# Performance work log

Hardware: AMD Instinct MI355X
Metric: run time of the kernel (lower is better)

The kernel has to match this reference:

```python
import jax, jax.numpy as jnp
import numpy as np

# Sizes: B graphs of N nodes each, K nearest neighbours, D=feat_dim=nhid, C=pos_dim
B, N, K, D, C = 4, 1024, 128, 32, 2
L = 3                     # number of EGNN conv layers
E_IN = 2 * D + 1          # edge MLP input: feats_i | feats_j | rel_dist (edge_dim=0, fourier=0)
E_H = 2 * E_IN            # edge MLP hidden


def _lin(key, fan_in, fan_out):
    kw, kb = jax.random.split(key)
    w = jax.random.normal(kw, (fan_in, fan_out), jnp.float32) / np.sqrt(fan_in)
    b = jax.random.normal(kb, (fan_out,), jnp.float32) * 0.01
    return w, b


def _stack(key, fan_in, fan_out):
    ws, bs = zip(*[_lin(k, fan_in, fan_out) for k in jax.random.split(key, L)])
    return jnp.stack(ws), jnp.stack(bs)


def setup_inputs() -> dict:
    key = jax.random.key(0)
    ks = jax.random.split(key, 10)
    feat_ = jax.random.normal(ks[0], (B * N, D), jnp.float32)
    coor_ = jax.random.normal(ks[1], (B * N, C), jnp.float32)
    batch = jnp.full((B,), N, dtype=jnp.int32)   # per-graph node counts (equal-size graphs)
    embed_w, embed_b = _lin(ks[2], D, D)         # embed: Linear(feat_dim, nhid)
    e1_w, e1_b = _stack(ks[3], E_IN, E_H)        # edge MLP
    e2_w, e2_b = _stack(ks[4], E_H, D)           # -> m_dim = nhid
    gate_w, gate_b = _stack(ks[5], D, 1)         # soft_edges gate
    c1_w, c1_b = _stack(ks[6], D, 4 * D)         # coors MLP
    c2_w, c2_b = _stack(ks[7], 4 * D, 1)
    n1_w, n1_b = _stack(ks[8], 2 * D, 2 * D)     # node MLP
    n2_w, n2_b = _stack(ks[9], 2 * D, D)
    coors_scale = jnp.full((L, 1), 1e-2, jnp.float32)  # CoorsNorm scale (init 1e-2)
    return dict(feat_=feat_, coor_=coor_, batch=batch, embed_w=embed_w, embed_b=embed_b,
                e1_w=e1_w, e1_b=e1_b, e2_w=e2_w, e2_b=e2_b, gate_w=gate_w, gate_b=gate_b,
                c1_w=c1_w, c1_b=c1_b, c2_w=c2_w, c2_b=c2_b, n1_w=n1_w, n1_b=n1_b,
                n2_w=n2_w, n2_b=n2_b, coors_scale=coors_scale)


def _lrelu(x):
    return jax.nn.leaky_relu(x, 0.1)


def _gather(x, idx):
    # x: [B, n, d], idx: [B, n, k] -> [B, n, k, d]
    return jax.vmap(lambda xb, ib: xb[ib])(x, idx)


def _egnn_layer(feats, coors, p):
    (e1_w, e1_b, e2_w, e2_b, gate_w, gate_b, c1_w, c1_b, c2_w, c2_b,
     n1_w, n1_b, n2_w, n2_b, scale) = p
    # pairwise squared distances; k smallest (self included, valid_radius=inf)
    diff = coors[:, :, None, :] - coors[:, None, :, :]      # [B,n,n,C]
    dist = jnp.sum(diff * diff, axis=-1)                    # [B,n,n]
    neg_d, idx = jax.lax.top_k(-dist, K)                    # k nearest
    rel_dist = -neg_d[..., None]                            # [B,n,K,1]
    rel_coors = coors[:, :, None, :] - _gather(coors, idx)  # [B,n,K,C]
    feats_j = _gather(feats, idx)                           # [B,n,K,D]
    feats_i = jnp.broadcast_to(feats[:, :, None, :], feats_j.shape)
    edge_in = jnp.concatenate([feats_i, feats_j, rel_dist], axis=-1)  # [B,n,K,E_IN]
    # edge MLP: Lin -> act -> Lin -> act ; soft edge gate
    m = _lrelu(_lrelu(edge_in @ e1_w + e1_b) @ e2_w + e2_b)            # [B,n,K,D]
    m = m * jax.nn.sigmoid(m @ gate_w + gate_b)
    # coordinate update: coors_mlp -> scalar weights; CoorsNorm on rel coords
    cw = (_lrelu(m @ c1_w + c1_b) @ c2_w + c2_b)[..., 0]               # [B,n,K]
    norm = jnp.maximum(jnp.linalg.norm(rel_coors, axis=-1, keepdims=True), 1e-8)
    rel_n = rel_coors / norm * scale
    coors_out = jnp.einsum('bik,bikc->bic', cw, rel_n) + coors
    # feature update: sum-pool messages, node MLP with residual
    m_i = jnp.sum(m, axis=2)                                           # [B,n,D]
    node_in = jnp.concatenate([feats, m_i], axis=-1)
    feats_out = _lrelu(node_in @ n1_w + n1_b) @ n2_w + n2_b + feats
    return feats_out, coors_out


def reference(feat_, coor_, batch, embed_w, embed_b, e1_w, e1_b, e2_w, e2_b,
              gate_w, gate_b, c1_w, c1_b, c2_w, c2_b, n1_w, n1_b, n2_w, n2_b,
              coors_scale):
    # embed MLP (dropout is identity at p=0 / eval), then batch equal-size graphs
    feats = _lrelu(feat_ @ embed_w + embed_b).reshape(B, N, D)
    coors = coor_.reshape(B, N, C)
    for l in range(L):
        p = (e1_w[l], e1_b[l], e2_w[l], e2_b[l], gate_w[l], gate_b[l],
             c1_w[l], c1_b[l], c2_w[l], c2_b[l], n1_w[l], n1_b[l],
             n2_w[l], n2_b[l], coors_scale[l])
        feats, coors = _egnn_layer(feats, coors, p)
    return feats.reshape(B * N, D)
```

## Files before the change

kernel.cpp:

```cpp
#include <hip/hip_runtime.h>
#include <hip/hip_bf16.h>
#include <math.h>

#define BB 4
#define NN 1024
#define KK 128
#define DD 32
#define LL 3
#define EH 130
#define EHP 132

typedef float f32x4 __attribute__((ext_vector_type(4)));
typedef short s16x8 __attribute__((ext_vector_type(8)));

__device__ __forceinline__ float lrelu(float x) { return fmaxf(x, 0.1f * x); }

__device__ __forceinline__ unsigned pk2(float a, float b) {
    __hip_bfloat162 h = __float22bfloat162_rn(float2{a, b});
    return *(unsigned*)&h;
}
__device__ __forceinline__ unsigned short bf16_hu(float v) {
    return (unsigned short)((__float_as_uint(v) + 0x8000u) >> 16);
}
__device__ __forceinline__ unsigned short bf16_rne(float v) {
    unsigned u = __float_as_uint(v);
    return (unsigned short)((u + 0x7fffu + ((u >> 16) & 1u)) >> 16);
}

__device__ __forceinline__ void knn_select(const float2* __restrict__ cbp, int i, int lane,
                                           unsigned* __restrict__ hist,
                                           int* __restrict__ nb) {
    const float2 ci = cbp[i];
    unsigned k[16];
#pragma unroll
    for (int s = 0; s < 16; s++) {
        float2 cj = cbp[lane + 64 * s];
        float dx = ci.x - cj.x, dy = ci.y - cj.y;
        float d = __fadd_rn(__fmul_rn(dx, dx), __fmul_rn(dy, dy));
        k[s] = __float_as_uint(d);
    }
    unsigned prefix = 0u;
    unsigned r = KK - 1;
#pragma unroll
    for (int pass = 0; pass < 4; pass++) {
        const int sh = 24 - 8 * pass;
        const unsigned mpref = (pass == 0) ? 0u : (0xFFFFFFFFu << (sh + 8));
        ((uint4*)hist)[lane] = uint4{0u, 0u, 0u, 0u};
        __threadfence_block();
#pragma unroll
        for (int s = 0; s < 16; s++) {
            if ((k[s] & mpref) == prefix)
                atomicAdd(&hist[(k[s] >> sh) & 255u], 1u);
        }
        __threadfence_block();
        const uint4 h = ((const uint4*)hist)[lane];
        const unsigned partial = h.x + h.y + h.z + h.w;
        unsigned incl = partial;
#pragma unroll
        for (int off = 1; off < 64; off <<= 1) {
            unsigned v = __shfl_up(incl, off, 64);
            if (lane >= off) incl += v;
        }
        const unsigned excl = incl - partial;
        const bool own = (r >= excl) && (r < incl);
        unsigned enc = 0u;
        if (own) {
            unsigned hh[4] = {h.x, h.y, h.z, h.w};
            unsigned e = excl;
            int bin = -1;
#pragma unroll
            for (int ii = 0; ii < 4; ii++) {
                if (bin < 0) {
                    if (r < e + hh[ii]) bin = ii;
                    else e += hh[ii];
                }
            }
            enc = (((unsigned)(4 * lane + bin)) << 16) | (r - e);
        }
        const unsigned long long mk = __ballot(own);
        const int src = __ffsll((unsigned long long)mk) - 1;
        enc = __shfl(enc, src, 64);
        prefix |= (enc >> 16) << sh;
        r = enc & 0xFFFFu;
    }
    const unsigned dstar = prefix;

    const unsigned long long below = (1ull << lane) - 1ull;
    unsigned run = 0;
#pragma unroll
    for (int s = 0; s < 16; s++) {
        unsigned long long m = __ballot(k[s] < dstar);
        if (k[s] < dstar) nb[run + (unsigned)__popcll(m & below)] = lane + 64 * s;
        run += (unsigned)__popcll(m);
    }
    const int need = KK - (int)run;
    unsigned tie = 0;
    for (int s = 0; s < 16 && (int)tie < need; s++) {
        unsigned long long m = __ballot(k[s] == dstar);
        if (k[s] == dstar) {
            unsigned r2 = tie + (unsigned)__popcll(m & below);
            if ((int)r2 < need) nb[run + r2] = lane + 64 * s;
        }
        tie += (unsigned)__popcll(m);
    }
}

__global__ __launch_bounds__(128) void prep_kernel(
    const float* __restrict__ feat,
    const float* __restrict__ ew, const float* __restrict__ eb,
    float* __restrict__ fout,
    const float* __restrict__ e1w0, const float* __restrict__ e1b0,
    float* __restrict__ HI, float* __restrict__ HJ,
    const float* __restrict__ e2w, const float* __restrict__ e2b,
    const float* __restrict__ c1w,
    unsigned short* __restrict__ e2f, unsigned short* __restrict__ c1f) {
    const int bid = blockIdx.x;
    const int t = threadIdx.x;
    if (bid < 2048) {
        __shared__ float sfe[2][DD];
        const int n0 = bid * 2;
        if (t < 64) {
            const int nl = t >> 5, o = t & 31;
            const float* f = feat + (size_t)(n0 + nl) * DD;
            float a = eb[o];
#pragma unroll
            for (int k = 0; k < DD; k++) a = fmaf(f[k], ew[k * DD + o], a);
            a = lrelu(a);
            fout[(size_t)(n0 + nl) * DD + o] = a;
            sfe[nl][o] = a;
        }
        __syncthreads();
        for (int idx = t; idx < 2 * EHP; idx += 128) {
            const int nl = idx / EHP, o = idx - nl * EHP;
            const size_t off = (size_t)(n0 + nl) * EHP + o;
            if (o >= EH) { HI[off] = 0.f; HJ[off] = 0.f; continue; }
            const float* fl = sfe[nl];
            float aa = e1b0[o], cc = 0.f;
#pragma unroll
            for (int k = 0; k < DD; k++) aa = fmaf(fl[k], e1w0[k * EH + o], aa);
#pragma unroll
            for (int k = 0; k < DD; k++) cc = fmaf(fl[k], e1w0[(DD + k) * EH + o], cc);
            HI[off] = aa;
            HJ[off] = cc;
        }
    } else {
        const int TOT_E2 = LL * 5120;
        const int TOT = TOT_E2 + LL * 4096;
        for (int u = (bid - 2048) * 128 + t; u < TOT; u += 96 * 128) {
            if (u < TOT_E2) {
                int l = u / 5120, v = u - l * 5120;
                int jj = v & 7, la = (v >> 3) & 63, nt = (v >> 9) & 1, c = v >> 10;
                int n = nt * 16 + (la & 15);
                float val;
                if (c < 4) {
                    int k = 32 * c + (la >> 4) * 8 + jj;
                    val = e2w[(size_t)l * EH * DD + k * DD + n];
                } else {
                    int ks = (la >> 4) * 8 + jj;
                    val = (ks == 0) ? e2w[((size_t)l * EH + 128) * DD + n]
                        : (ks == 1) ? e2w[((size_t)l * EH + 129) * DD + n]
                        : (ks == 2) ? e2b[(size_t)l * DD + n] : 0.f;
                }
                e2f[u] = bf16_rne(val);
            } else {
                int v = u - TOT_E2;
                int jj = v & 7, la = (v >> 3) & 63, nt = (v >> 9) & 7, l = v >> 12;
                int k = (la >> 4) * 8 + jj;
                int n = nt * 16 + (la & 15);
                c1f[v] = bf16_rne(c1w[(size_t)l * DD * 128 + k * 128 + n]);
            }
        }
    }
}

__global__ __launch_bounds__(256) void layer_kernel(
    const float* __restrict__ feats_in, const float* __restrict__ coors_in,
    const float* __restrict__ HI, const float* __restrict__ HJ,
    const float* __restrict__ w65,
    const unsigned short* __restrict__ e2f,
    const unsigned short* __restrict__ c1f,
    const float* __restrict__ gw, const float* __restrict__ gb,
    const float* __restrict__ c1b, const float* __restrict__ c2w, const float* __restrict__ c2b,
    const float* __restrict__ n1w, const float* __restrict__ n1b,
    const float* __restrict__ n2w, const float* __restrict__ n2b,
    const float* __restrict__ scale,
    const float* __restrict__ e1wn, const float* __restrict__ e1bn,
    float* __restrict__ HIn, float* __restrict__ HJn,
    float* __restrict__ feats_out, float* __restrict__ coors_out) {
    const int node = blockIdx.x;
    const int b = node >> 10;
    const int t = threadIdx.x;
    const int lane = t & 63, wid = t >> 6;
    const int ln = lane & 15, q = lane >> 4;
    const int rowbase = wid * 32;

    __shared__ __align__(16) float shi[EHP];
    __shared__ __align__(16) float sw65[EHP];
    __shared__ __align__(16) unsigned short smA[4 * 32 * 32];
    __shared__ float sx0[128], sx1[128], su[128], sv[128], srd[128];
    __shared__ int snb[128];
    __shared__ float sgw[DD], sfi[DD], sfo[DD];
    __shared__ float sc1b[128], sc2w[128];
    __shared__ float redm[4][DD], redc[4][2];
    __shared__ float sni[2 * DD], shd[2 * DD];
    __shared__ float sp1[4][2 * DD], sp2[4][DD];

    if (t < 64) {
        knn_select((const float2*)coors_in + (size_t)b * NN, node & (NN - 1), lane,
                   (unsigned*)smA, snb);
    } else {
        for (int u = t - 64; u < EHP; u += 192) {
            shi[u] = HI[(size_t)node * EHP + u];
            sw65[u] = (u < EH) ? w65[u] : 0.f;
        }
        if (t - 64 < DD) { sfi[t - 64] = feats_in[node * DD + (t - 64)]; sgw[t - 64] = gw[t - 64]; }
        if (t >= 128) { sc1b[t - 128] = c1b[t - 128]; sc2w[t - 128] = c2w[t - 128]; }
    }
    __syncthreads();

    const float cix = coors_in[node * 2], ciy = coors_in[node * 2 + 1];
    if (t < 128) {
        const int j = snb[t];
        const float2 cj = *(const float2*)(coors_in + ((size_t)(b * NN) + j) * 2);
        const float dx = cix - cj.x, dy = ciy - cj.y;
        const float rd = __fadd_rn(__fmul_rn(dx, dx), __fmul_rn(dy, dy));
        srd[t] = rd;
        const float nrm = fmaxf(sqrtf(rd), 1e-8f);
        const float s = scale[0] / nrm;
        su[t] = dx * s;
        sv[t] = dy * s;
        const float2 hjt = *(const float2*)(HJ + ((size_t)(b * NN) + j) * EHP + 128);
        sx0[t] = lrelu(shi[128] + hjt.x + rd * sw65[128]);
        sx1[t] = lrelu(shi[129] + hjt.y + rd * sw65[129]);
    }
    __syncthreads();

    float rdR[2];
    const float* hjb[2];
#pragma unroll
    for (int mt = 0; mt < 2; mt++) {
        const int row = rowbase + mt * 16 + ln;
        rdR[mt] = srd[row];
        hjb[mt] = HJ + ((size_t)(b * NN) + snb[row]) * EHP;
    }

    const float4* shi4 = (const float4*)shi;
    const float4* sw4  = (const float4*)sw65;

    const f32x4 zz = {0.f, 0.f, 0.f, 0.f};
    f32x4 accA[2][2];
    accA[0][0] = zz; accA[0][1] = zz; accA[1][0] = zz; accA[1][1] = zz;

    float4 ha[2], hbv[2];
#pragma unroll
    for (int mt = 0; mt < 2; mt++) {
        const float4* hjp = (const float4*)(hjb[mt] + q * 8);
        ha[mt] = hjp[0];
        hbv[mt] = hjp[1];
    }
    s16x8 bcur0 = *(const s16x8*)(e2f + (0 * 64 + lane) * 8);
    s16x8 bcur1 = *(const s16x8*)(e2f + (1 * 64 + lane) * 8);

#pragma unroll 1
    for (int c = 0; c < 4; c++) {
        s16x8 bn0 = *(const s16x8*)(e2f + (((c + 1) * 2 + 0) * 64 + lane) * 8);
        s16x8 bn1 = *(const s16x8*)(e2f + (((c + 1) * 2 + 1) * 64 + lane) * 8);
        float4 nha[2], nhb[2];
        if (c < 3) {
#pragma unroll
            for (int mt = 0; mt < 2; mt++) {
                const float4* hjp = (const float4*)(hjb[mt] + (c + 1) * 32 + q * 8);
                nha[mt] = hjp[0];
                nhb[mt] = hjp[1];
            }
        }
        const int kb = c * 8 + q * 2;
        const float4 hi0 = shi4[kb], hi1 = shi4[kb + 1];
        const float4 wv0 = sw4[kb],  wv1 = sw4[kb + 1];
#pragma unroll
        for (int mt = 0; mt < 2; mt++) {
            const float r = rdR[mt];
            union { s16x8 v; unsigned u[4]; } A;
            A.u[0] = pk2(lrelu(hi0.x + ha[mt].x + r * wv0.x), lrelu(hi0.y + ha[mt].y + r * wv0.y));
            A.u[1] = pk2(lrelu(hi0.z + ha[mt].z + r * wv0.z), lrelu(hi0.w + ha[mt].w + r * wv0.w));
            A.u[2] = pk2(lrelu(hi1.x + hbv[mt].x + r * wv1.x), lrelu(hi1.y + hbv[mt].y + r * wv1.y));
            A.u[3] = pk2(lrelu(hi1.z + hbv[mt].z + r * wv1.z), lrelu(hi1.w + hbv[mt].w + r * wv1.w));
            accA[mt][0] = __builtin_amdgcn_mfma_f32_16x16x32_bf16(A.v, bcur0, accA[mt][0], 0, 0, 0);
            accA[mt][1] = __builtin_amdgcn_mfma_f32_16x16x32_bf16(A.v, bcur1, accA[mt][1], 0, 0, 0);
        }
#pragma unroll
        for (int mt = 0; mt < 2; mt++) { ha[mt] = nha[mt]; hbv[mt] = nhb[mt]; }
        bcur0 = bn0; bcur1 = bn1;
    }

    {
#pragma unroll
        for (int mt = 0; mt < 2; mt++) {
            const int row = rowbase + mt * 16 + ln;
            union { s16x8 v; unsigned u[4]; } A;
            const unsigned p0 = pk2(sx0[row], sx1[row]);
            A.u[0] = (q == 0) ? p0 : 0u;
            A.u[1] = (q == 0) ? 0x00003f80u : 0u;
            A.u[2] = 0u;
            A.u[3] = 0u;
            accA[mt][0] = __builtin_amdgcn_mfma_f32_16x16x32_bf16(A.v, bcur0, accA[mt][0], 0, 0, 0);
            accA[mt][1] = __builtin_amdgcn_mfma_f32_16x16x32_bf16(A.v, bcur1, accA[mt][1], 0, 0, 0);
        }
    }

    s16x8 cfr[8];
#pragma unroll
    for (int g8 = 0; g8 < 8; g8++)
        cfr[g8] = *(const s16x8*)(c1f + (g8 * 64 + lane) * 8);

#pragma unroll
    for (int mt = 0; mt < 2; mt++)
#pragma unroll
        for (int nt = 0; nt < 2; nt++)
#pragma unroll
            for (int r = 0; r < 4; r++)
                accA[mt][nt][r] = lrelu(accA[mt][nt][r]);

    const float gbv = gb[0];
#pragma unroll
    for (int mt = 0; mt < 2; mt++) {
        float p[4];
#pragma unroll
        for (int r = 0; r < 4; r++)
            p[r] = accA[mt][0][r] * sgw[ln] + accA[mt][1][r] * sgw[16 + ln];
#pragma unroll
        for (int off = 1; off <= 8; off <<= 1)
#pragma unroll
            for (int r = 0; r < 4; r++) p[r] += __shfl_xor(p[r], off);
#pragma unroll
        for (int r = 0; r < 4; r++) {
            const float g = 1.f / (1.f + __expf(-(p[r] + gbv)));
            accA[mt][0][r] *= g;
            accA[mt][1][r] *= g;
        }
    }

    float mi0 = 0.f, mi1 = 0.f;
#pragma unroll
    for (int mt = 0; mt < 2; mt++)
#pragma unroll
        for (int r = 0; r < 4; r++) { mi0 += accA[mt][0][r]; mi1 += accA[mt][1][r]; }
    mi0 += __shfl_xor(mi0, 16); mi0 += __shfl_xor(mi0, 32);
    mi1 += __shfl_xor(mi1, 16); mi1 += __shfl_xor(mi1, 32);
    if (lane < 16) { redm[wid][lane] = mi0; redm[wid][16 + lane] = mi1; }

    __syncthreads();
    unsigned short* smw = smA + wid * (32 * 32);
#pragma unroll
    for (int mt = 0; mt < 2; mt++)
#pragma unroll
        for (int nt = 0; nt < 2; nt++)
#pragma unroll
            for (int r = 0; r < 4; r++) {
                const int prow = (r << 3) | (4 * mt + q);
                smw[prow * 32 + nt * 16 + ln] = bf16_hu(accA[mt][nt][r]);
            }

    s16x8 a4[2];
#pragma unroll
    for (int mt = 0; mt < 2; mt++) {
        const int prow = ((ln & 3) << 3) | (4 * mt + (ln >> 2));
        a4[mt] = *(const s16x8*)(smw + prow * 32 + q * 8);
    }

    float cacc[2][4];
#pragma unroll
    for (int mt = 0; mt < 2; mt++)
#pragma unroll
        for (int r = 0; r < 4; r++) cacc[mt][r] = 0.f;

#pragma unroll
    for (int g = 0; g < 4; g++) {
        const float cb0 = sc1b[(2 * g + 0) * 16 + ln];
        const float cb1 = sc1b[(2 * g + 1) * 16 + ln];
        const f32x4 ci0 = {cb0, cb0, cb0, cb0};
        const f32x4 ci1 = {cb1, cb1, cb1, cb1};
        f32x4 c20[2], c21[2];
#pragma unroll
        for (int mt = 0; mt < 2; mt++) {
            c20[mt] = __builtin_amdgcn_mfma_f32_16x16x32_bf16(a4[mt], cfr[2 * g + 0], ci0, 0, 0, 0);
            c21[mt] = __builtin_amdgcn_mfma_f32_16x16x32_bf16(a4[mt], cfr[2 * g + 1], ci1, 0, 0, 0);
        }
#pragma unroll
        for (int h = 0; h < 2; h++) {
            const float c2wv = sc2w[(2 * g + h) * 16 + ln];
#pragma unroll
            for (int mt = 0; mt < 2; mt++)
#pragma unroll
                for (int r = 0; r < 4; r++) {
                    const float v = (h ? c21[mt][r] : c20[mt][r]);
                    cacc[mt][r] = fmaf(lrelu(v), c2wv, cacc[mt][r]);
                }
        }
    }
#pragma unroll
    for (int off = 1; off <= 8; off <<= 1)
#pragma unroll
        for (int mt = 0; mt < 2; mt++)
#pragma unroll
            for (int r = 0; r < 4; r++) cacc[mt][r] += __shfl_xor(cacc[mt][r], off);

    const float c2bv = c2b[0];
    float vxp = 0.f, vyp = 0.f;
    if (ln == 0) {
#pragma unroll
        for (int mt = 0; mt < 2; mt++)
#pragma unroll
            for (int r = 0; r < 4; r++) {
                const int row = rowbase + mt * 16 + q * 4 + r;
                const float cw = cacc[mt][r] + c2bv;
                vxp = fmaf(cw, su[row], vxp);
                vyp = fmaf(cw, sv[row], vyp);
            }
    }
    vxp += __shfl_xor(vxp, 16); vxp += __shfl_xor(vxp, 32);
    vyp += __shfl_xor(vyp, 16); vyp += __shfl_xor(vyp, 32);
    if (lane == 0) { redc[wid][0] = vxp; redc[wid][1] = vyp; }

    __syncthreads();
    if (t < DD) {
        sni[t] = sfi[t];
        sni[DD + t] = redm[0][t] + redm[1][t] + redm[2][t] + redm[3][t];
    }
    __syncthreads();
    {
        const int o = t & 63, p = t >> 6;
        float a = 0.f;
#pragma unroll
        for (int k = 0; k < 16; k++) a = fmaf(sni[p * 16 + k], n1w[(p * 16 + k) * 64 + o], a);
        sp1[p][o] = a;
    }
    __syncthreads();
    if (t < 2 * DD)
        shd[t] = lrelu(n1b[t] + ((sp1[0][t] + sp1[1][t]) + (sp1[2][t] + sp1[3][t])));
    __syncthreads();
    if (t < 128) {
        const int o = t & 31, p = t >> 5;
        float a = 0.f;
#pragma unroll
        for (int k = 0; k < 16; k++) a = fmaf(shd[p * 16 + k], n2w[(p * 16 + k) * DD + o], a);
        sp2[p][o] = a;
    }
    __syncthreads();
    if (t < DD) {
        const float val = n2b[t] + ((sp2[0][t] + sp2[1][t]) + (sp2[2][t] + sp2[3][t])) + sfi[t];
        feats_out[node * DD + t] = val;
        sfo[t] = val;
    }
    if (t == 0) {
        coors_out[node * 2]     = cix + redc[0][0] + redc[1][0] + redc[2][0] + redc[3][0];
        coors_out[node * 2 + 1] = ciy + redc[0][1] + redc[1][1] + redc[2][1] + redc[3][1];
    }
    __syncthreads();

    if (e1wn) {
        for (int idx = t; idx < 2 * EHP; idx += 256) {
            const int nl = idx / EHP, o = idx - nl * EHP;
            float* dst = (nl ? HJn : HIn) + (size_t)node * EHP + o;
            if (o >= EH) { *dst = 0.f; continue; }
            const int rowoff = nl ? DD : 0;
            float a = nl ? 0.f : e1bn[o];
#pragma unroll
            for (int k = 0; k < DD; k++) a = fmaf(sfo[k], e1wn[(rowoff + k) * EH + o], a);
            *dst = a;
        }
    }
}

extern "C" void kernel_launch(void* const* d_in, const int* in_sizes, int n_in,
                              void* d_out, int out_size, void* d_ws, size_t ws_size,
                              hipStream_t stream) {
    const float* feat_   = (const float*)d_in[0];
    const float* coor_   = (const float*)d_in[1];
    const float* embed_w = (const float*)d_in[3];
    const float* embed_b = (const float*)d_in[4];
    const float* e1_w    = (const float*)d_in[5];
    const float* e1_b    = (const float*)d_in[6];
    const float* e2_w    = (const float*)d_in[7];
    const float* e2_b    = (const float*)d_in[8];
    const float* gate_w  = (const float*)d_in[9];
    const float* gate_b  = (const float*)d_in[10];
    const float* c1_w    = (const float*)d_in[11];
    const float* c1_b    = (const float*)d_in[12];
    const float* c2_w    = (const float*)d_in[13];
    const float* c2_b    = (const float*)d_in[14];
    const float* n1_w    = (const float*)d_in[15];
    const float* n1_b    = (const float*)d_in[16];
    const float* n2_w    = (const float*)d_in[17];
    const float* n2_b    = (const float*)d_in[18];
    const float* cscale  = (const float*)d_in[19];

    float* ws = (float*)d_ws;
    float* fa   = ws;   ws += BB * NN * DD;
    float* fb   = ws;   ws += BB * NN * DD;
    float* ca   = ws;   ws += BB * NN * 2;
    float* cb2  = ws;   ws += BB * NN * 2;
    float* HI0  = ws;   ws += BB * NN * EHP;
    float* HJ0  = ws;   ws += BB * NN * EHP;
    float* HI1  = ws;   ws += BB * NN * EHP;
    float* HJ1  = ws;   ws += BB * NN * EHP;
    unsigned short* e2f = (unsigned short*)ws;
    unsigned short* c1f = e2f + LL * 5120;

    prep_kernel<<<2048 + 96, 128, 0, stream>>>(feat_, embed_w, embed_b, fa,
                                               e1_w, e1_b, HI0, HJ0,
                                               e2_w, e2_b, c1_w, e2f, c1f);

    float* HIbuf[2] = {HI0, HI1};
    float* HJbuf[2] = {HJ0, HJ1};
    const float* fin = fa;
    const float* cin = coor_;
    float* fouts[LL] = {fb, fa, (float*)d_out};
    float* couts[LL] = {ca, cb2, ca};

    for (int l = 0; l < LL; l++) {
        const int cur = l & 1, nxt = (l + 1) & 1;
        layer_kernel<<<BB * NN, 256, 0, stream>>>(
            fin, cin, HIbuf[cur], HJbuf[cur],
            e1_w + ((size_t)l * 65 + 64) * EH,
            e2f + (size_t)l * 5120,
            c1f + (size_t)l * 4096,
            gate_w + (size_t)l * DD,
            gate_b + l,
            c1_b + (size_t)l * 128,
            c2_w + (size_t)l * 128,
            c2_b + l,
            n1_w + (size_t)l * 64 * 64,
            n1_b + (size_t)l * 64,
            n2_w + (size_t)l * 64 * 32,
            n2_b + (size_t)l * DD,
            cscale + l,
            (l < LL - 1) ? (e1_w + (size_t)(l + 1) * 65 * EH) : nullptr,
            (l < LL - 1) ? (e1_b + (size_t)(l + 1) * EH) : nullptr,
            HIbuf[nxt], HJbuf[nxt],
            fouts[l], couts[l]);
        fin = fouts[l];
        cin = couts[l];
    }
}
```

Before: 328.7 us.

## Spread kNN radix selection across all four waves of the block

```diff
diff --git a/kernel.cpp b/kernel.cpp
--- a/kernel.cpp
+++ b/kernel.cpp
@@ -27,14 +27,17 @@
     return (unsigned short)((u + 0x7fffu + ((u >> 16) & 1u)) >> 16);
 }
 
-__device__ __forceinline__ void knn_select(const float2* __restrict__ cbp, int i, int lane,
-                                           unsigned* __restrict__ hist,
-                                           int* __restrict__ nb) {
+__device__ __forceinline__ void knn_block(const float2* __restrict__ cbp, int i, int t,
+                                          unsigned* __restrict__ hist,
+                                          volatile unsigned* __restrict__ scr,
+                                          int* __restrict__ nb) {
+    const int lane = t & 63, wid = t >> 6;
+    unsigned* histw = hist + wid * 256;
     const float2 ci = cbp[i];
-    unsigned k[16];
-#pragma unroll
-    for (int s = 0; s < 16; s++) {
-        float2 cj = cbp[lane + 64 * s];
+    unsigned k[4];
+#pragma unroll
+    for (int s = 0; s < 4; s++) {
+        float2 cj = cbp[wid * 256 + s * 64 + lane];
         float dx = ci.x - cj.x, dy = ci.y - cj.y;
         float d = __fadd_rn(__fmul_rn(dx, dx), __fmul_rn(dy, dy));
         k[s] = __float_as_uint(d);
@@ -45,63 +48,69 @@
     for (int pass = 0; pass < 4; pass++) {
         const int sh = 24 - 8 * pass;
         const unsigned mpref = (pass == 0) ? 0u : (0xFFFFFFFFu << (sh + 8));
-        ((uint4*)hist)[lane] = uint4{0u, 0u, 0u, 0u};
-        __threadfence_block();
-#pragma unroll
-        for (int s = 0; s < 16; s++) {
+        ((uint4*)histw)[lane] = uint4{0u, 0u, 0u, 0u};
+#pragma unroll
+        for (int s = 0; s < 4; s++) {
             if ((k[s] & mpref) == prefix)
-                atomicAdd(&hist[(k[s] >> sh) & 255u], 1u);
-        }
-        __threadfence_block();
-        const uint4 h = ((const uint4*)hist)[lane];
-        const unsigned partial = h.x + h.y + h.z + h.w;
-        unsigned incl = partial;
+                atomicAdd(&histw[(k[s] >> sh) & 255u], 1u);
+        }
+        __syncthreads();
+        unsigned tot = hist[t] + hist[256 + t] + hist[512 + t] + hist[768 + t];
+        unsigned incl = tot;
 #pragma unroll
         for (int off = 1; off < 64; off <<= 1) {
             unsigned v = __shfl_up(incl, off, 64);
             if (lane >= off) incl += v;
         }
-        const unsigned excl = incl - partial;
-        const bool own = (r >= excl) && (r < incl);
-        unsigned enc = 0u;
-        if (own) {
-            unsigned hh[4] = {h.x, h.y, h.z, h.w};
-            unsigned e = excl;
-            int bin = -1;
-#pragma unroll
-            for (int ii = 0; ii < 4; ii++) {
-                if (bin < 0) {
-                    if (r < e + hh[ii]) bin = ii;
-                    else e += hh[ii];
-                }
-            }
-            enc = (((unsigned)(4 * lane + bin)) << 16) | (r - e);
-        }
-        const unsigned long long mk = __ballot(own);
-        const int src = __ffsll((unsigned long long)mk) - 1;
-        enc = __shfl(enc, src, 64);
-        prefix |= (enc >> 16) << sh;
-        r = enc & 0xFFFFu;
+        if (lane == 63) scr[wid] = incl;
+        __syncthreads();
+        unsigned woff = 0;
+#pragma unroll
+        for (int w = 0; w < 4; w++)
+            if (w < wid) woff += scr[w];
+        incl += woff;
+        const unsigned excl = incl - tot;
+        if (r >= excl && r < incl) { scr[4] = (unsigned)t; scr[5] = r - excl; }
+        __syncthreads();
+        prefix |= scr[4] << sh;
+        r = scr[5];
     }
     const unsigned dstar = prefix;
 
     const unsigned long long below = (1ull << lane) - 1ull;
-    unsigned run = 0;
-#pragma unroll
-    for (int s = 0; s < 16; s++) {
-        unsigned long long m = __ballot(k[s] < dstar);
-        if (k[s] < dstar) nb[run + (unsigned)__popcll(m & below)] = lane + 64 * s;
-        run += (unsigned)__popcll(m);
-    }
-    const int need = KK - (int)run;
-    unsigned tie = 0;
-    for (int s = 0; s < 16 && (int)tie < need; s++) {
-        unsigned long long m = __ballot(k[s] == dstar);
+    unsigned long long mL[4], mE[4];
+    unsigned cntL = 0, cntE = 0;
+#pragma unroll
+    for (int s = 0; s < 4; s++) {
+        mL[s] = __ballot(k[s] < dstar);
+        mE[s] = __ballot(k[s] == dstar);
+        cntL += (unsigned)__popcll(mL[s]);
+        cntE += (unsigned)__popcll(mE[s]);
+    }
+    if (lane == 0) { scr[8 + wid] = cntL; scr[12 + wid] = cntE; }
+    __syncthreads();
+    unsigned offL = 0, offE = 0, totalL = 0;
+#pragma unroll
+    for (int w = 0; w < 4; w++) {
+        unsigned cl = scr[8 + w];
+        if (w < wid) { offL += cl; offE += scr[12 + w]; }
+        totalL += cl;
+    }
+    unsigned run = offL;
+#pragma unroll
+    for (int s = 0; s < 4; s++) {
+        if (k[s] < dstar) nb[run + (unsigned)__popcll(mL[s] & below)] = wid * 256 + s * 64 + lane;
+        run += (unsigned)__popcll(mL[s]);
+    }
+    const int need = KK - (int)totalL;
+    unsigned tie = offE;
+#pragma unroll
+    for (int s = 0; s < 4; s++) {
         if (k[s] == dstar) {
-            unsigned r2 = tie + (unsigned)__popcll(m & below);
-            if ((int)r2 < need) nb[run + r2] = lane + 64 * s;
-        }
-        tie += (unsigned)__popcll(m);
+            unsigned r2 = tie + (unsigned)__popcll(mE[s] & below);
+            if ((int)r2 < need) nb[totalL + r2] = wid * 256 + s * 64 + lane;
+        }
+        tie += (unsigned)__popcll(mE[s]);
     }
 }
 
@@ -197,6 +206,7 @@
     __shared__ __align__(16) float shi[EHP];
     __shared__ __align__(16) float sw65[EHP];
     __shared__ __align__(16) unsigned short smA[4 * 32 * 32];
+    __shared__ unsigned sknn[16];
     __shared__ float sx0[128], sx1[128], su[128], sv[128], srd[128];
     __shared__ int snb[128];
     __shared__ float sgw[DD], sfi[DD], sfo[DD];
@@ -205,17 +215,15 @@
     __shared__ float sni[2 * DD], shd[2 * DD];
     __shared__ float sp1[4][2 * DD], sp2[4][DD];
 
-    if (t < 64) {
-        knn_select((const float2*)coors_in + (size_t)b * NN, node & (NN - 1), lane,
-                   (unsigned*)smA, snb);
-    } else {
-        for (int u = t - 64; u < EHP; u += 192) {
-            shi[u] = HI[(size_t)node * EHP + u];
-            sw65[u] = (u < EH) ? w65[u] : 0.f;
-        }
-        if (t - 64 < DD) { sfi[t - 64] = feats_in[node * DD + (t - 64)]; sgw[t - 64] = gw[t - 64]; }
-        if (t >= 128) { sc1b[t - 128] = c1b[t - 128]; sc2w[t - 128] = c2w[t - 128]; }
-    }
+    for (int u = t; u < EHP; u += 256) {
+        shi[u] = HI[(size_t)node * EHP + u];
+        sw65[u] = (u < EH) ? w65[u] : 0.f;
+    }
+    if (t < DD) { sfi[t] = feats_in[node * DD + t]; sgw[t] = gw[t]; }
+    if (t >= 128) { sc1b[t - 128] = c1b[t - 128]; sc2w[t - 128] = c2w[t - 128]; }
+
+    knn_block((const float2*)coors_in + (size_t)b * NN, node & (NN - 1), t,
+              (unsigned*)smA, sknn, snb);
     __syncthreads();
 
     const float cix = coors_in[node * 2], ciy = coors_in[node * 2 + 1];
@@ -349,7 +357,6 @@
     mi1 += __shfl_xor(mi1, 16); mi1 += __shfl_xor(mi1, 32);
     if (lane < 16) { redm[wid][lane] = mi0; redm[wid][16 + lane] = mi1; }
 
-    __syncthreads();
     unsigned short* smw = smA + wid * (32 * 32);
 #pragma unroll
     for (int mt = 0; mt < 2; mt++)
```

New measurement: 316.8 us. -3.6%, faster.
